# Optimization experiments

Hardware: AMD Instinct MI355X
Metric: run time of the kernel (lower is better)

The kernel has to match this reference:

```python
import jax, jax.numpy as jnp
import numpy as np

N, E, DIN, H, HEADS = 50000, 800000, 128, 64, 4


def setup_inputs() -> dict:
    key = jax.random.key(0)
    ks = jax.random.split(key, 12)

    def p(k, shape, fan_in):
        return jax.random.normal(k, shape, dtype=jnp.float32) / np.float32(np.sqrt(fan_in))

    return dict(
        x=jax.random.normal(ks[0], (N, DIN), dtype=jnp.float32),
        edge_index=jax.random.randint(ks[1], (2, E), 0, N, dtype=jnp.int32),
        # GCNConv(input_dim, hidden)
        W_gcn=p(ks[2], (DIN, H), DIN), b_gcn=jnp.zeros((H,), jnp.float32),
        # GATConv(hidden, hidden, heads=4, concat=True)
        W_gat=p(ks[3], (H, HEADS * H), H),
        att_src=p(ks[4], (HEADS, H), H), att_dst=p(ks[5], (HEADS, H), H),
        b_gat=jnp.zeros((HEADS * H,), jnp.float32),
        # SAGEConv(4*hidden, hidden): lin_l (neighbors, with bias), lin_r (root, no bias)
        W_sage_l=p(ks[6], (HEADS * H, H), HEADS * H), b_sage=jnp.zeros((H,), jnp.float32),
        W_sage_r=p(ks[7], (HEADS * H, H), HEADS * H),
        # edge-pair MLP: Linear(2*hidden, hidden) -> ReLU -> Linear(hidden, 1)
        W1=p(ks[8], (2 * H, H), 2 * H), b1=jnp.zeros((H,), jnp.float32),
        W2=p(ks[9], (H, 1), H), b2=jnp.zeros((1,), jnp.float32),
    )


def reference(x, edge_index, W_gcn, b_gcn, W_gat, att_src, att_dst, b_gat,
              W_sage_l, b_sage, W_sage_r, W1, b1, W2, b2):
    n = x.shape[0]
    src, dst = edge_index[0], edge_index[1]
    loop = jnp.arange(n, dtype=edge_index.dtype)
    # edges with self-loops appended (GCN and GAT add self-loops by default)
    s2 = jnp.concatenate([src, loop])
    d2 = jnp.concatenate([dst, loop])

    h = x @ W_gcn                                            # [N, H]
    deg = jax.ops.segment_sum(jnp.ones_like(d2, jnp.float32), d2, num_segments=n)
    dinv = jnp.where(deg > 0, jax.lax.rsqrt(jnp.maximum(deg, 1e-12)), 0.0)
    norm = dinv[s2] * dinv[d2]                               # [E+N]
    h = jax.ops.segment_sum(h[s2] * norm[:, None], d2, num_segments=n) + b_gcn
    h = jax.nn.relu(h)                                       # dropout: identity in eval

    # ---- GATConv (heads=4, concat=True, negative_slope=0.2) ----
    g = (h @ W_gat).reshape(n, HEADS, H)                     # [N, heads, C]
    a_s = jnp.sum(g * att_src, axis=-1)                      # [N, heads]
    a_d = jnp.sum(g * att_dst, axis=-1)
    e = jax.nn.leaky_relu(a_s[s2] + a_d[d2], 0.2)            # [E+N, heads]
    m = jax.ops.segment_max(e, d2, num_segments=n)           # per-target max (stable softmax)
    e = jnp.exp(e - m[d2])
    z = jax.ops.segment_sum(e, d2, num_segments=n)
    alpha = e / (z[d2] + 1e-16)                              # edge softmax over incoming edges
    g = jax.ops.segment_sum(g[s2] * alpha[:, :, None], d2, num_segments=n)
    g = jax.nn.relu(g.reshape(n, HEADS * H) + b_gat)

    # ---- SAGEConv (mean aggregation, root weight, no self-loops) ----
    nsum = jax.ops.segment_sum(g[src], dst, num_segments=n)
    cnt = jax.ops.segment_sum(jnp.ones_like(dst, jnp.float32), dst, num_segments=n)
    mean = nsum / jnp.maximum(cnt, 1.0)[:, None]
    s = jax.nn.relu(mean @ W_sage_l + b_sage + g @ W_sage_r)  # [N, H]

    # ---- edge-pair MLP + sigmoid ----
    ef = jnp.concatenate([s[src], s[dst]], axis=1)            # [E, 2H]
    pred = jax.nn.relu(ef @ W1 + b1) @ W2 + b2                # [E, 1]
    return jax.nn.sigmoid(pred[:, 0])
```

## Files before the change

### kernel.cpp

```cpp
#include <hip/hip_runtime.h>
#include <math.h>

typedef float v2f __attribute__((ext_vector_type(2)));
static __device__ __forceinline__ float4 f4s(float v){ return make_float4(v,v,v,v); }
static __device__ __forceinline__ float4 f4add(float4 a, float4 b){ return make_float4(a.x+b.x,a.y+b.y,a.z+b.z,a.w+b.w); }
static __device__ __forceinline__ float4 f4max(float4 a, float4 b){ return make_float4(fmaxf(a.x,b.x),fmaxf(a.y,b.y),fmaxf(a.z,b.z),fmaxf(a.w,b.w)); }
static __device__ __forceinline__ float4 f4scale(float4 a, float s){ return make_float4(a.x*s,a.y*s,a.z*s,a.w*s); }
static __device__ __forceinline__ float4 f4fma(float4 acc, float s, float4 b){
  acc.x += s*b.x; acc.y += s*b.y; acc.z += s*b.z; acc.w += s*b.w; return acc;
}
static __device__ __forceinline__ float4 f4relu(float4 a){ return f4max(a, f4s(0.f)); }
static __device__ __forceinline__ float4 f4leaky(float4 a){
  return make_float4(a.x>0.f?a.x:0.2f*a.x, a.y>0.f?a.y:0.2f*a.y, a.z>0.f?a.z:0.2f*a.z, a.w>0.f?a.w:0.2f*a.w);
}
static __device__ __forceinline__ float4 f4expf(float4 a){ return make_float4(__expf(a.x),__expf(a.y),__expf(a.z),__expf(a.w)); }
static __device__ __forceinline__ unsigned short f2bf(float f){
  unsigned int u = __float_as_uint(f);
  unsigned int r = (u + 0x7fffu + ((u >> 16) & 1u)) >> 16;
  return (unsigned short)r;
}
static __device__ __forceinline__ ushort4 f2bf4(float4 f){
  ushort4 r; r.x=f2bf(f.x); r.y=f2bf(f.y); r.z=f2bf(f.z); r.w=f2bf(f.w); return r;
}
static __device__ __forceinline__ float4 bfu2f4(uint2 u){
  return make_float4(__uint_as_float(u.x << 16), __uint_as_float(u.x & 0xffff0000u),
                     __uint_as_float(u.y << 16), __uint_as_float(u.y & 0xffff0000u));
}
static __device__ __forceinline__ float4 bfu2f4_lo(uint4 u){ return bfu2f4(make_uint2(u.x, u.y)); }
static __device__ __forceinline__ float4 bfu2f4_hi(uint4 u){ return bfu2f4(make_uint2(u.z, u.w)); }

typedef __attribute__((ext_vector_type(8))) unsigned short u16x8;
static __device__ __forceinline__ u16x8 f2bf8(float4 a, float4 b){
  u16x8 r;
  r[0]=f2bf(a.x); r[1]=f2bf(a.y); r[2]=f2bf(a.z); r[3]=f2bf(a.w);
  r[4]=f2bf(b.x); r[5]=f2bf(b.y); r[6]=f2bf(b.z); r[7]=f2bf(b.w);
  return r;
}
static __device__ __forceinline__ void red2(float4& a, float4& b){
  a.x += __shfl_xor(a.x, 8); a.y += __shfl_xor(a.y, 8);
  a.z += __shfl_xor(a.z, 8); a.w += __shfl_xor(a.w, 8);
  b.x += __shfl_xor(b.x, 8); b.y += __shfl_xor(b.y, 8);
  b.z += __shfl_xor(b.z, 8); b.w += __shfl_xor(b.w, 8);
}
static __device__ __forceinline__ unsigned char f2fp8(float v){
  return (unsigned char)(__builtin_amdgcn_cvt_pk_fp8_f32(v, v, 0, false) & 0xff);
}
static __device__ __forceinline__ unsigned int f4_fp8x4(float4 v){
  unsigned int r = __builtin_amdgcn_cvt_pk_fp8_f32(v.x, v.y, 0, false);
  r = __builtin_amdgcn_cvt_pk_fp8_f32(v.z, v.w, r, true);
  return r;
}
static __device__ __forceinline__ float4 fp8x4_f4(unsigned int q){
  v2f lo = __builtin_amdgcn_cvt_pk_f32_fp8(q, false);
  v2f hi = __builtin_amdgcn_cvt_pk_f32_fp8(q, true);
  return make_float4(lo[0], lo[1], hi[0], hi[1]);
}
static __device__ __forceinline__ float dot8(float4 a, float4 b, const float* v){
  return a.x*v[0]+a.y*v[1]+a.z*v[2]+a.w*v[3]+b.x*v[4]+b.y*v[5]+b.z*v[6]+b.w*v[7];
}

typedef __attribute__((ext_vector_type(8))) short bf16x8;
typedef __attribute__((ext_vector_type(4))) float f32x4;

__global__ __launch_bounds__(256) void k_rankw(const int* __restrict__ dst, int* __restrict__ cnt,
                                               int* __restrict__ rank, int E, int fb,
                                               const float* __restrict__ Wg, const float* __restrict__ Wl,
                                               const float* __restrict__ Wr, unsigned short* __restrict__ WT){
  if ((int)blockIdx.x < fb){
    int t = blockIdx.x*256 + threadIdx.x;
    if (t < E) rank[t] = atomicAdd(&cnt[dst[t]], 1);
    return;
  }
  int s = (blockIdx.x - fb)*256 + threadIdx.x;
  int l = s & 63, f = s >> 6;
  const float* wp; int ld;
  if (s < 2048){
    int cc = f & 15, kb = f >> 4;
    int c  = cc*16 + (l & 15);
    int kr = kb*32 + ((l >> 4) << 3);
    wp = Wg + (size_t)kr*256 + c; ld = 256;
  } else {
    int f2 = f - 32;
    int cc = f2 & 7, kb = f2 >> 3;
    int c  = cc*16 + (l & 15);
    int kr = kb*32 + ((l >> 4) << 3);
    wp = (c >= 64) ? (Wr + (size_t)kr*64 + (c - 64)) : (Wl + (size_t)kr*64 + c);
    ld = 64;
  }
  u16x8 o;
  #pragma unroll
  for (int j = 0; j < 8; ++j) o[j] = f2bf(wp[(size_t)j*ld]);
  *(u16x8*)(WT + (size_t)s*8) = o;
}

__global__ __launch_bounds__(256) void k_scan1v(const int* __restrict__ cnt, int* __restrict__ excl,
                                                int* __restrict__ bsum, int n, int nb,
                                                const float* __restrict__ Wg, const float* __restrict__ as,
                                                const float* __restrict__ ad, float* __restrict__ Vs,
                                                float* __restrict__ Vd){
  if ((int)blockIdx.x == nb){
    int t = threadIdx.x;
    int h = t >> 6, k = t & 63;
    float s = 0.f, d = 0.f;
    const float* wr = Wg + (size_t)k*256 + h*64;
    const float* ar = as + h*64;
    const float* dr = ad + h*64;
    for (int c = 0; c < 64; ++c){ float w = wr[c]; s += w*ar[c]; d += w*dr[c]; }
    Vs[t] = s; Vd[t] = d;
    return;
  }
  __shared__ int sc[256];
  int t = threadIdx.x; int i = blockIdx.x*256 + t;
  int v = (i<n)?cnt[i]:0;
  sc[t]=v; __syncthreads();
  for (int o=1;o<256;o<<=1){ int a=(t>=o)?sc[t-o]:0; __syncthreads(); sc[t]+=a; __syncthreads(); }
  if (i<n) excl[i] = sc[t]-v;
  if (t==255) bsum[blockIdx.x] = sc[t];
}
__global__ __launch_bounds__(256) void k_scan3b(const int* __restrict__ cnt, const int* __restrict__ excl,
                                                const int* __restrict__ bsum, int* __restrict__ offs,
                                                float* __restrict__ dinv, int n, int E, int nb){
  __shared__ int sb[256];
  int t = threadIdx.x;
  int v = (t<nb)?bsum[t]:0;
  sb[t]=v; __syncthreads();
  for (int o=1;o<256;o<<=1){ int a=(t>=o)?sb[t-o]:0; __syncthreads(); sb[t]+=a; __syncthreads(); }
  int bex = sb[blockIdx.x] - bsum[blockIdx.x];
  int i = blockIdx.x*256 + t;
  if (i < n){
    offs[i] = excl[i] + bex;
    dinv[i] = rsqrtf((float)cnt[i] + 1.0f);
    if (i == 0) offs[n] = E;
  }
}

__global__ __launch_bounds__(256) void k_fillg(const int* __restrict__ src, const int* __restrict__ dstv,
                                               const int* __restrict__ offs, const int* __restrict__ rank,
                                               int* __restrict__ csr, int E, int fb,
                                               const float* __restrict__ x, const float* __restrict__ Wg,
                                               unsigned char* __restrict__ a8, int n,
                                               const float* __restrict__ dinv){
  if ((int)blockIdx.x < fb){
    int t = blockIdx.x*256 + threadIdx.x;
    if (t < E) csr[offs[dstv[t]] + rank[t]] = src[t];
    return;
  }
  __shared__ unsigned short wb[1024*8];
  int tid = threadIdx.x;
  for (int s = tid; s < 1024; s += 256){
    int l = s & 63, f = s >> 6;
    int cc = f & 3, kb = f >> 2;
    int c  = cc*16 + (l & 15);
    int kr = kb*32 + ((l >> 4) << 3);
    const float* wp = Wg + (size_t)kr*64 + c;
    unsigned short* dp = &wb[s*8];
    #pragma unroll
    for (int j = 0; j < 8; ++j) dp[j] = f2bf(wp[(size_t)j*64]);
  }
  __syncthreads();
  int wv = tid >> 6, l = tid & 63;
  int lrow = l & 15;
  int lk = (l >> 4) << 3;
  int g = blockIdx.x - fb;
  int r0 = (g << 6) + (wv << 4);
  int m = r0 + lrow;
  bf16x8 afr[4];
  #pragma unroll
  for (int kb = 0; kb < 4; ++kb){
    bf16x8 a = {0,0,0,0,0,0,0,0};
    if (m < n){
      const float* p = x + (size_t)m*128 + kb*32 + lk;
      float4 f0 = *(const float4*)p;
      float4 f1 = *(const float4*)(p + 4);
      a[0]=(short)f2bf(f0.x); a[1]=(short)f2bf(f0.y); a[2]=(short)f2bf(f0.z); a[3]=(short)f2bf(f0.w);
      a[4]=(short)f2bf(f1.x); a[5]=(short)f2bf(f1.y); a[6]=(short)f2bf(f1.z); a[7]=(short)f2bf(f1.w);
    }
    afr[kb] = a;
  }
  int rbase = r0 + ((l >> 4) << 2);
  float sc[4];
  #pragma unroll
  for (int r = 0; r < 4; ++r) sc[r] = (rbase + r < n) ? dinv[rbase + r] : 0.f;
  #pragma unroll
  for (int cc = 0; cc < 4; ++cc){
    f32x4 acc = {0.f, 0.f, 0.f, 0.f};
    #pragma unroll
    for (int kb = 0; kb < 4; ++kb){
      bf16x8 b = *(const bf16x8*)&wb[((kb*4 + cc)*64 + l)*8];
      acc = __builtin_amdgcn_mfma_f32_16x16x32_bf16(afr[kb], b, acc, 0, 0, 0);
    }
    int c = cc*16 + lrow;
    #pragma unroll
    for (int r = 0; r < 4; ++r){
      int rr = rbase + r;
      if (rr < n) a8[(size_t)rr*64 + c] = f2fp8(acc[r] * sc[r]);
    }
  }
}

__global__ __launch_bounds__(256) void k_gcn(const unsigned char* __restrict__ a8, const float* __restrict__ dinv,
                                             const float* __restrict__ b, const int* __restrict__ offs,
                                             const int* __restrict__ csr, const float* __restrict__ Vs,
                                             const float* __restrict__ Vd, unsigned char* __restrict__ h8,
                                             float* __restrict__ D, int n){
  __shared__ float svs[256], svd[256];
  svs[threadIdx.x] = Vs[threadIdx.x];
  svd[threadIdx.x] = Vd[threadIdx.x];
  __syncthreads();
  int l = threadIdx.x & 63;
  int node = (((blockIdx.x*256 + threadIdx.x) >> 6) << 2) + (l >> 4);
  int l15 = l & 15;
  int grp = l15 >> 3, sub = l15 & 7;
  bool ok = node < n;
  int beg = 0, end = 0;
  float di = 0.f;
  if (ok){ beg = offs[node]; end = offs[node+1]; di = dinv[node]; }
  float4 aL0 = f4s(0.f), aH0 = f4s(0.f), aL1 = f4s(0.f), aH1 = f4s(0.f);
  int i = beg + grp;
  for (; i + 2 < end; i += 4){
    int s0 = csr[i], s1 = csr[i+2];
    uint2 u0 = *(const uint2*)(a8 + (size_t)s0*64 + (sub<<3));
    uint2 u1 = *(const uint2*)(a8 + (size_t)s1*64 + (sub<<3));
    aL0 = f4add(aL0, fp8x4_f4(u0.x)); aH0 = f4add(aH0, fp8x4_f4(u0.y));
    aL1 = f4add(aL1, fp8x4_f4(u1.x)); aH1 = f4add(aH1, fp8x4_f4(u1.y));
  }
  if (i < end){
    int s0 = csr[i];
    uint2 u0 = *(const uint2*)(a8 + (size_t)s0*64 + (sub<<3));
    aL0 = f4add(aL0, fp8x4_f4(u0.x)); aH0 = f4add(aH0, fp8x4_f4(u0.y));
  }
  float4 aL = f4add(aL0, aL1), aH = f4add(aH0, aH1);
  red2(aL, aH);
  if (ok){
    uint2 us = *(const uint2*)(a8 + (size_t)node*64 + (sub<<3));
    aL = f4add(aL, fp8x4_f4(us.x)); aH = f4add(aH, fp8x4_f4(us.y));
    float4 b0 = *(const float4*)(b + (sub<<3));
    float4 b1 = *(const float4*)(b + (sub<<3) + 4);
    float4 r0 = f4relu(f4fma(b0, di, aL));
    float4 r1 = f4relu(f4fma(b1, di, aH));
    if (grp == 0){
      uint2 q; q.x = f4_fp8x4(r0); q.y = f4_fp8x4(r1);
      *(uint2*)(h8 + (size_t)node*64 + (sub<<3)) = q;
    }
    const float* vs0 = svs + (grp*128) + (sub<<3);
    const float* vd0 = svd + (grp*128) + (sub<<3);
    float s0 = dot8(r0, r1, vs0);
    float s1 = dot8(r0, r1, vs0 + 64);
    float d0 = dot8(r0, r1, vd0);
    float d1 = dot8(r0, r1, vd0 + 64);
    #pragma unroll
    for (int o = 1; o < 8; o <<= 1){
      s0 += __shfl_xor(s0, o); s1 += __shfl_xor(s1, o);
      d0 += __shfl_xor(d0, o); d1 += __shfl_xor(d1, o);
    }
    if (sub == 0){
      *(float2*)(D + (size_t)node*8 + grp*2)     = make_float2(s0, s1);
      *(float2*)(D + (size_t)node*8 + 4 + grp*2) = make_float2(d0, d1);
    }
  }
}

#define GAT_CAP 128
__global__ __launch_bounds__(256) void k_gat2f(const float* __restrict__ D, const unsigned char* __restrict__ H8,
                                               const int* __restrict__ offs, const int* __restrict__ csr,
                                               const unsigned short* __restrict__ WT, const float* __restrict__ bg,
                                               unsigned short* __restrict__ R, unsigned char* __restrict__ P8, int n){
  __shared__ float wl[8][GAT_CAP*4];
  __shared__ int   sl[8][GAT_CAP];
  __shared__ unsigned short ytile[16][264];
  unsigned short* gtile = (unsigned short*)&wl[0][0];
  const unsigned short* WT1 = WT;
  const unsigned short* WT2 = WT + 2048*8;
  int tid = threadIdx.x;
  for (int s0 = tid; s0 < 8*264; s0 += 256) (&ytile[8][0])[s0] = 0;
  int hw = tid >> 5;
  int node = (blockIdx.x*256 + tid) >> 5;
  int l5 = tid & 31;
  int grp = l5 >> 4;
  int sub = l5 & 15;
  if (node < n){
    int beg = offs[node], end = offs[node+1];
    int deg = end - beg;
    float4 ed  = *(const float4*)(D + (size_t)node*8 + 4);
    float4 es0 = *(const float4*)(D + (size_t)node*8);
    float4 wself = f4expf(f4leaky(f4add(es0, ed)));
    float4 z4 = f4s(0.f);
    for (int i = beg + l5; i < end; i += 32){
      int s = csr[i];
      float4 w = f4expf(f4leaky(f4add(*(const float4*)(D + (size_t)s*8), ed)));
      int li = i - beg;
      if (li < GAT_CAP){ *(float4*)&wl[hw][li<<2] = w; sl[hw][li] = s << 6; }
      z4 = f4add(z4, w);
    }
    for (int m = 1; m < 32; m <<= 1){
      z4.x += __shfl_xor(z4.x, m); z4.y += __shfl_xor(z4.y, m);
      z4.z += __shfl_xor(z4.z, m); z4.w += __shfl_xor(z4.w, m);
    }
    z4 = f4add(z4, wself);
    int c0b = sub << 2;
    float4 a0 = f4s(0.f), a1 = f4s(0.f), a2 = f4s(0.f), a3 = f4s(0.f);
    int nl = deg < GAT_CAP ? deg : GAT_CAP;
    int i = grp;
    for (; i + 2 < nl; i += 4){
      int o0 = sl[hw][i], o1 = sl[hw][i+2];
      float4 w0 = *(const float4*)&wl[hw][i<<2];
      float4 w1 = *(const float4*)&wl[hw][(i+2)<<2];
      unsigned int q0 = *(const unsigned int*)(H8 + o0 + c0b);
      unsigned int q1 = *(const unsigned int*)(H8 + o1 + c0b);
      float4 f0 = fp8x4_f4(q0);
      float4 f1 = fp8x4_f4(q1);
      a0 = f4fma(a0, w0.x, f0); a1 = f4fma(a1, w0.y, f0);
      a2 = f4fma(a2, w0.z, f0); a3 = f4fma(a3, w0.w, f0);
      a0 = f4fma(a0, w1.x, f1); a1 = f4fma(a1, w1.y, f1);
      a2 = f4fma(a2, w1.z, f1); a3 = f4fma(a3, w1.w, f1);
    }
    if (i < nl){
      float4 w0 = *(const float4*)&wl[hw][i<<2];
      float4 f0 = fp8x4_f4(*(const unsigned int*)(H8 + sl[hw][i] + c0b));
      a0 = f4fma(a0, w0.x, f0); a1 = f4fma(a1, w0.y, f0);
      a2 = f4fma(a2, w0.z, f0); a3 = f4fma(a3, w0.w, f0);
    }
    for (int j = nl + grp; j < deg; j += 2){
      int s = csr[beg+j];
      float4 e = f4leaky(f4add(*(const float4*)(D + (size_t)s*8), ed));
      float4 w = f4expf(e);
      float4 f0 = fp8x4_f4(*(const unsigned int*)(H8 + ((size_t)s << 6) + c0b));
      a0 = f4fma(a0, w.x, f0); a1 = f4fma(a1, w.y, f0);
      a2 = f4fma(a2, w.z, f0); a3 = f4fma(a3, w.w, f0);
    }
    a0.x += __shfl_xor(a0.x, 16); a0.y += __shfl_xor(a0.y, 16); a0.z += __shfl_xor(a0.z, 16); a0.w += __shfl_xor(a0.w, 16);
    a1.x += __shfl_xor(a1.x, 16); a1.y += __shfl_xor(a1.y, 16); a1.z += __shfl_xor(a1.z, 16); a1.w += __shfl_xor(a1.w, 16);
    a2.x += __shfl_xor(a2.x, 16); a2.y += __shfl_xor(a2.y, 16); a2.z += __shfl_xor(a2.z, 16); a2.w += __shfl_xor(a2.w, 16);
    a3.x += __shfl_xor(a3.x, 16); a3.y += __shfl_xor(a3.y, 16); a3.z += __shfl_xor(a3.z, 16); a3.w += __shfl_xor(a3.w, 16);
    if (grp == 0){
      float4 fs = fp8x4_f4(*(const unsigned int*)(H8 + ((size_t)node << 6) + c0b));
      a0 = f4fma(a0, wself.x, fs);
      a1 = f4fma(a1, wself.y, fs);
      a2 = f4fma(a2, wself.z, fs);
      a3 = f4fma(a3, wself.w, fs);
      a0 = f4scale(a0, 1.f/(z4.x + 1e-16f));
      a1 = f4scale(a1, 1.f/(z4.y + 1e-16f));
      a2 = f4scale(a2, 1.f/(z4.z + 1e-16f));
      a3 = f4scale(a3, 1.f/(z4.w + 1e-16f));
      unsigned short* yp = &ytile[hw][sub << 2];
      *(ushort4*)(yp)       = f2bf4(a0);
      *(ushort4*)(yp + 64)  = f2bf4(a1);
      *(ushort4*)(yp + 128) = f2bf4(a2);
      *(ushort4*)(yp + 192) = f2bf4(a3);
    }
  } else if (grp == 0){
    ushort4 z = make_ushort4(0,0,0,0);
    unsigned short* yp = &ytile[hw][sub << 2];
    *(ushort4*)(yp)       = z;
    *(ushort4*)(yp + 64)  = z;
    *(ushort4*)(yp + 128) = z;
    *(ushort4*)(yp + 192) = z;
  }
  __syncthreads();
  int wv = tid >> 6, l = tid & 63;
  int lrow = l & 15;
  int lk = (l >> 4) << 3;
  int rbase4 = (l >> 4) << 2;
  bf16x8 af0 = *(const bf16x8*)&ytile[lrow][wv*64 + lk];
  bf16x8 af1 = *(const bf16x8*)&ytile[lrow][wv*64 + 32 + lk];
  #pragma unroll
  for (int q = 0; q < 4; ++q){
    int cc = wv*4 + q;
    f32x4 acc = {0.f, 0.f, 0.f, 0.f};
    acc = __builtin_amdgcn_mfma_f32_16x16x32_bf16(af0, *(const bf16x8*)&WT1[((size_t)((0*16 + cc)*64 + l))*8], acc, 0, 0, 0);
    acc = __builtin_amdgcn_mfma_f32_16x16x32_bf16(af1, *(const bf16x8*)&WT1[((size_t)((1*16 + cc)*64 + l))*8], acc, 0, 0, 0);
    int c = cc*16 + lrow;
    float bv = bg[c];
    #pragma unroll
    for (int r = 0; r < 4; ++r)
      gtile[(rbase4 + r)*264 + c] = f2bf(fmaxf(acc[r] + bv, 0.f));
  }
  __syncthreads();
  bf16x8 afb[8];
  #pragma unroll
  for (int kb = 0; kb < 8; ++kb)
    afb[kb] = *(const bf16x8*)&gtile[lrow*264 + kb*32 + lk];
  #pragma unroll
  for (int q = 0; q < 2; ++q){
    int cc = wv*2 + q;
    f32x4 acc = {0.f, 0.f, 0.f, 0.f};
    #pragma unroll
    for (int kb = 0; kb < 8; ++kb){
      bf16x8 b = *(const bf16x8*)&WT2[((size_t)((kb*8 + cc)*64 + l))*8];
      acc = __builtin_amdgcn_mfma_f32_16x16x32_bf16(afb[kb], b, acc, 0, 0, 0);
    }
    int c = cc*16 + lrow;
    #pragma unroll
    for (int r = 0; r < 4; ++r){
      int row = rbase4 + r;
      if (row < 8){
        int nd = blockIdx.x*8 + row;
        if (nd < n){
          float v = acc[r];
          if (c < 64) P8[(size_t)nd*64 + c] = f2fp8(v);
          else        R[(size_t)nd*64 + (c - 64)] = f2bf(v);
        }
      }
    }
  }
}

__global__ __launch_bounds__(256) void k_sage(const unsigned char* __restrict__ P8, const unsigned short* __restrict__ R,
                                              const float* __restrict__ b, const int* __restrict__ offs,
                                              const int* __restrict__ csr, const float* __restrict__ W1a,
                                              const float* __restrict__ W1b, unsigned char* __restrict__ T2, int n){
  __shared__ unsigned short wfr[1024*8];
  __shared__ unsigned short stile[16][72];
  int tid = threadIdx.x;
  for (int s = tid; s < 1024; s += 256){
    int l = s & 63, f = s >> 6;
    int cc = f & 7, kb = f >> 3;
    int c  = cc*16 + (l & 15);
    int kr = kb*32 + ((l >> 4) << 3);
    const float* wp = (c >= 64) ? (W1b + (size_t)kr*64 + (c - 64)) : (W1a + (size_t)kr*64 + c);
    unsigned short* dp = &wfr[s*8];
    #pragma unroll
    for (int j = 0; j < 8; ++j) dp[j] = f2bf(wp[(size_t)j*64]);
  }
  int wv = tid >> 6, l = tid & 63;
  int base = blockIdx.x*16;
  int lrow16 = (wv << 2) + (l >> 4);
  int node = base + lrow16;
  int l15 = l & 15;
  int grp = l15 >> 3, sub = l15 & 7;
  bool ok = node < n;
  int beg = 0, end = 0;
  if (ok){ beg = offs[node]; end = offs[node+1]; }
  float4 aL0 = f4s(0.f), aH0 = f4s(0.f), aL1 = f4s(0.f), aH1 = f4s(0.f);
  int i = beg + grp;
  for (; i + 2 < end; i += 4){
    int s0 = csr[i], s1 = csr[i+2];
    uint2 u0 = *(const uint2*)(P8 + (size_t)s0*64 + (sub<<3));
    uint2 u1 = *(const uint2*)(P8 + (size_t)s1*64 + (sub<<3));
    aL0 = f4add(aL0, fp8x4_f4(u0.x)); aH0 = f4add(aH0, fp8x4_f4(u0.y));
    aL1 = f4add(aL1, fp8x4_f4(u1.x)); aH1 = f4add(aH1, fp8x4_f4(u1.y));
  }
  if (i < end){
    int s0 = csr[i];
    uint2 u0 = *(const uint2*)(P8 + (size_t)s0*64 + (sub<<3));
    aL0 = f4add(aL0, fp8x4_f4(u0.x)); aH0 = f4add(aH0, fp8x4_f4(u0.y));
  }
  float4 aL = f4add(aL0, aL1), aH = f4add(aH0, aH1);
  red2(aL, aH);
  float4 r0 = f4s(0.f), r1 = f4s(0.f);
  if (ok){
    float minv = 1.f / fmaxf((float)(end - beg), 1.f);
    uint4 ur = *(const uint4*)(R + (size_t)node*64 + (sub<<3));
    float4 b0 = *(const float4*)(b + (sub<<3));
    float4 b1 = *(const float4*)(b + (sub<<3) + 4);
    r0 = f4relu(f4add(f4fma(b0, minv, aL), bfu2f4_lo(ur)));
    r1 = f4relu(f4add(f4fma(b1, minv, aH), bfu2f4_hi(ur)));
  }
  if (grp == 0) *(u16x8*)&stile[lrow16][sub << 3] = f2bf8(r0, r1);
  __syncthreads();
  int lrow = l & 15, lk = (l >> 4) << 3;
  bf16x8 af0 = *(const bf16x8*)&stile[lrow][lk];
  bf16x8 af1 = *(const bf16x8*)&stile[lrow][32 + lk];
  int rbase = (l >> 4) << 2;
  #pragma unroll
  for (int q = 0; q < 2; ++q){
    int cc = wv*2 + q;
    f32x4 acc = {0.f, 0.f, 0.f, 0.f};
    acc = __builtin_amdgcn_mfma_f32_16x16x32_bf16(af0, *(const bf16x8*)&wfr[(cc*64 + l)*8], acc, 0, 0, 0);
    acc = __builtin_amdgcn_mfma_f32_16x16x32_bf16(af1, *(const bf16x8*)&wfr[((8 + cc)*64 + l)*8], acc, 0, 0, 0);
    int c = cc*16 + lrow;
    #pragma unroll
    for (int r = 0; r < 4; ++r){
      int nd = base + rbase + r;
      if (nd < n) T2[(size_t)nd*128 + c] = f2fp8(acc[r]);
    }
  }
}

__global__ __launch_bounds__(256) void k_mlp(const unsigned char* __restrict__ T2,
                                             const float* __restrict__ b1, const float* __restrict__ W2,
                                             const float* __restrict__ b2, const int* __restrict__ src,
                                             const int* __restrict__ dst, float* __restrict__ out, int E){
  int t = threadIdx.x;
  int e = blockIdx.x*32 + (t >> 3);
  if (e >= E) return;
  int sub = t & 7;
  int s = src[e], d = dst[e];
  uint2 uu = *(const uint2*)(T2 + (size_t)s*128 + (sub<<3));
  uint2 vv = *(const uint2*)(T2 + (size_t)d*128 + 64 + (sub<<3));
  float4 u0 = fp8x4_f4(uu.x), u1 = fp8x4_f4(uu.y);
  float4 v0 = fp8x4_f4(vv.x), v1 = fp8x4_f4(vv.y);
  float4 bb0 = *(const float4*)(b1 + (sub<<3));
  float4 bb1 = *(const float4*)(b1 + (sub<<3) + 4);
  float4 w0 = *(const float4*)(W2 + (sub<<3));
  float4 w1 = *(const float4*)(W2 + (sub<<3) + 4);
  float4 ta = f4relu(f4add(f4add(u0, v0), bb0));
  float4 tb = f4relu(f4add(f4add(u1, v1), bb1));
  float p = ta.x*w0.x + ta.y*w0.y + ta.z*w0.z + ta.w*w0.w
          + tb.x*w1.x + tb.y*w1.y + tb.z*w1.z + tb.w*w1.w;
  p += __shfl_xor(p, 1);
  p += __shfl_xor(p, 2);
  p += __shfl_xor(p, 4);
  if (sub == 0) out[e] = 1.f / (1.f + __expf(-(p + b2[0])));
}

extern "C" void kernel_launch(void* const* d_in, const int* in_sizes, int n_in,
                              void* d_out, int out_size, void* d_ws, size_t ws_size,
                              hipStream_t stream){
  const float* x     = (const float*)d_in[0];
  const int*   eidx  = (const int*)  d_in[1];
  const float* W_gcn = (const float*)d_in[2];
  const float* b_gcn = (const float*)d_in[3];
  const float* W_gat = (const float*)d_in[4];
  const float* att_s = (const float*)d_in[5];
  const float* att_d = (const float*)d_in[6];
  const float* b_gat = (const float*)d_in[7];
  const float* W_sl  = (const float*)d_in[8];
  const float* b_sg  = (const float*)d_in[9];
  const float* W_sr  = (const float*)d_in[10];
  const float* W1    = (const float*)d_in[11];
  const float* b1    = (const float*)d_in[12];
  const float* W2    = (const float*)d_in[13];
  const float* b2    = (const float*)d_in[14];
  float* out = (float*)d_out;

  const int N = in_sizes[0] / 128;
  const int E = in_sizes[1] / 2;
  const int* src = eidx;
  const int* dst = eidx + E;

  float* ws   = (float*)d_ws;
  float* dinv = ws;
  float* D    = dinv + (size_t)N;
  float* Vs   = D + (size_t)N*8;
  float* Vd   = Vs + 256;
  unsigned short* WT = (unsigned short*)(Vd + 256);
  unsigned short* R  = WT + (size_t)6144*8;
  unsigned char*  A8 = (unsigned char*)(R + (size_t)N*64);
  unsigned char*  H8 = A8 + (size_t)N*64;
  unsigned char*  P8 = H8 + (size_t)N*64;
  unsigned char*  T2 = P8 + (size_t)N*64;
  int* cnt  = (int*)(T2 + (size_t)N*128);
  int* excl = cnt + N;
  int* bsum = excl + N;
  int* offs = bsum + 256;
  int* rank = offs + N + 1;
  int* csr  = rank + E;

  const int nb = (N + 255) / 256;
  const int fb = (E + 255) / 256;
  const int gtiles = (N + 63) / 64;
  const int nwb = (N + 15) / 16;

  hipMemsetAsync(cnt, 0, (size_t)N*sizeof(int), stream);
  k_rankw <<<fb + 24, 256, 0, stream>>>(dst, cnt, rank, E, fb, W_gat, W_sl, W_sr, WT);
  k_scan1v<<<nb + 1, 256, 0, stream>>>(cnt, excl, bsum, N, nb, W_gat, att_s, att_d, Vs, Vd);
  k_scan3b<<<nb, 256, 0, stream>>>(cnt, excl, bsum, offs, dinv, N, E, nb);
  k_fillg <<<fb + gtiles, 256, 0, stream>>>(src, dst, offs, rank, csr, E, fb,
                                            x, W_gcn, A8, N, dinv);

  k_gcn <<<nwb, 256, 0, stream>>>(A8, dinv, b_gcn, offs, csr, Vs, Vd, H8, D, N);

  k_gat2f<<<(N+7)/8, 256, 0, stream>>>(D, H8, offs, csr, WT, b_gat, R, P8, N);

  k_sage<<<nwb, 256, 0, stream>>>(P8, R, b_sg, offs, csr, W1, W1 + 64*64, T2, N);

  k_mlp <<<(E+31)/32, 256, 0, stream>>>(T2, b1, W2, b2, src, dst, out, E);
}
```

Before: 276.1 us.

## Process 32 nodes per GAT block to fill MFMA tiles and reuse weights

The fused GAT kernel now aggregates 32 nodes per block, with each half-wave handling four nodes in sequence, instead of 8. The two following MFMA projections then run on two full 16-row tiles rather than one half-padded tile. Each weight fragment loaded from global memory is reused across both tiles, and the zero-padding waste and per-block weight traffic drop by a factor of four. In exchange the grid has fewer blocks, the serialized aggregation makes each block longer, and the larger ytile plus extra register fragments may lower occupancy.

```diff
diff --git a/kernel.cpp b/kernel.cpp
--- a/kernel.cpp
+++ b/kernel.cpp
@@ -265,136 +265,153 @@
                                                const int* __restrict__ offs, const int* __restrict__ csr,
                                                const unsigned short* __restrict__ WT, const float* __restrict__ bg,
                                                unsigned short* __restrict__ R, unsigned char* __restrict__ P8, int n){
-  __shared__ float wl[8][GAT_CAP*4];
-  __shared__ int   sl[8][GAT_CAP];
-  __shared__ unsigned short ytile[16][264];
-  unsigned short* gtile = (unsigned short*)&wl[0][0];
+  __shared__ __align__(16) unsigned char smem_raw[8*GAT_CAP*4*4 + 8*GAT_CAP*4];
+  __shared__ unsigned short ytile[32][264];
+  float (*wl)[GAT_CAP*4] = reinterpret_cast<float (*)[GAT_CAP*4]>(smem_raw);
+  int   (*sl)[GAT_CAP]   = reinterpret_cast<int (*)[GAT_CAP]>(smem_raw + 8*GAT_CAP*4*4);
+  unsigned short* gtile  = reinterpret_cast<unsigned short*>(smem_raw);
   const unsigned short* WT1 = WT;
   const unsigned short* WT2 = WT + 2048*8;
   int tid = threadIdx.x;
-  for (int s0 = tid; s0 < 8*264; s0 += 256) (&ytile[8][0])[s0] = 0;
   int hw = tid >> 5;
-  int node = (blockIdx.x*256 + tid) >> 5;
   int l5 = tid & 31;
   int grp = l5 >> 4;
   int sub = l5 & 15;
-  if (node < n){
-    int beg = offs[node], end = offs[node+1];
-    int deg = end - beg;
-    float4 ed  = *(const float4*)(D + (size_t)node*8 + 4);
-    float4 es0 = *(const float4*)(D + (size_t)node*8);
-    float4 wself = f4expf(f4leaky(f4add(es0, ed)));
-    float4 z4 = f4s(0.f);
-    for (int i = beg + l5; i < end; i += 32){
-      int s = csr[i];
-      float4 w = f4expf(f4leaky(f4add(*(const float4*)(D + (size_t)s*8), ed)));
-      int li = i - beg;
-      if (li < GAT_CAP){ *(float4*)&wl[hw][li<<2] = w; sl[hw][li] = s << 6; }
-      z4 = f4add(z4, w);
-    }
-    for (int m = 1; m < 32; m <<= 1){
-      z4.x += __shfl_xor(z4.x, m); z4.y += __shfl_xor(z4.y, m);
-      z4.z += __shfl_xor(z4.z, m); z4.w += __shfl_xor(z4.w, m);
-    }
-    z4 = f4add(z4, wself);
-    int c0b = sub << 2;
-    float4 a0 = f4s(0.f), a1 = f4s(0.f), a2 = f4s(0.f), a3 = f4s(0.f);
-    int nl = deg < GAT_CAP ? deg : GAT_CAP;
-    int i = grp;
-    for (; i + 2 < nl; i += 4){
-      int o0 = sl[hw][i], o1 = sl[hw][i+2];
-      float4 w0 = *(const float4*)&wl[hw][i<<2];
-      float4 w1 = *(const float4*)&wl[hw][(i+2)<<2];
-      unsigned int q0 = *(const unsigned int*)(H8 + o0 + c0b);
-      unsigned int q1 = *(const unsigned int*)(H8 + o1 + c0b);
-      float4 f0 = fp8x4_f4(q0);
-      float4 f1 = fp8x4_f4(q1);
-      a0 = f4fma(a0, w0.x, f0); a1 = f4fma(a1, w0.y, f0);
-      a2 = f4fma(a2, w0.z, f0); a3 = f4fma(a3, w0.w, f0);
-      a0 = f4fma(a0, w1.x, f1); a1 = f4fma(a1, w1.y, f1);
-      a2 = f4fma(a2, w1.z, f1); a3 = f4fma(a3, w1.w, f1);
-    }
-    if (i < nl){
-      float4 w0 = *(const float4*)&wl[hw][i<<2];
-      float4 f0 = fp8x4_f4(*(const unsigned int*)(H8 + sl[hw][i] + c0b));
-      a0 = f4fma(a0, w0.x, f0); a1 = f4fma(a1, w0.y, f0);
-      a2 = f4fma(a2, w0.z, f0); a3 = f4fma(a3, w0.w, f0);
-    }
-    for (int j = nl + grp; j < deg; j += 2){
-      int s = csr[beg+j];
-      float4 e = f4leaky(f4add(*(const float4*)(D + (size_t)s*8), ed));
-      float4 w = f4expf(e);
-      float4 f0 = fp8x4_f4(*(const unsigned int*)(H8 + ((size_t)s << 6) + c0b));
-      a0 = f4fma(a0, w.x, f0); a1 = f4fma(a1, w.y, f0);
-      a2 = f4fma(a2, w.z, f0); a3 = f4fma(a3, w.w, f0);
-    }
-    a0.x += __shfl_xor(a0.x, 16); a0.y += __shfl_xor(a0.y, 16); a0.z += __shfl_xor(a0.z, 16); a0.w += __shfl_xor(a0.w, 16);
-    a1.x += __shfl_xor(a1.x, 16); a1.y += __shfl_xor(a1.y, 16); a1.z += __shfl_xor(a1.z, 16); a1.w += __shfl_xor(a1.w, 16);
-    a2.x += __shfl_xor(a2.x, 16); a2.y += __shfl_xor(a2.y, 16); a2.z += __shfl_xor(a2.z, 16); a2.w += __shfl_xor(a2.w, 16);
-    a3.x += __shfl_xor(a3.x, 16); a3.y += __shfl_xor(a3.y, 16); a3.z += __shfl_xor(a3.z, 16); a3.w += __shfl_xor(a3.w, 16);
-    if (grp == 0){
-      float4 fs = fp8x4_f4(*(const unsigned int*)(H8 + ((size_t)node << 6) + c0b));
-      a0 = f4fma(a0, wself.x, fs);
-      a1 = f4fma(a1, wself.y, fs);
-      a2 = f4fma(a2, wself.z, fs);
-      a3 = f4fma(a3, wself.w, fs);
-      a0 = f4scale(a0, 1.f/(z4.x + 1e-16f));
-      a1 = f4scale(a1, 1.f/(z4.y + 1e-16f));
-      a2 = f4scale(a2, 1.f/(z4.z + 1e-16f));
-      a3 = f4scale(a3, 1.f/(z4.w + 1e-16f));
-      unsigned short* yp = &ytile[hw][sub << 2];
-      *(ushort4*)(yp)       = f2bf4(a0);
-      *(ushort4*)(yp + 64)  = f2bf4(a1);
-      *(ushort4*)(yp + 128) = f2bf4(a2);
-      *(ushort4*)(yp + 192) = f2bf4(a3);
-    }
-  } else if (grp == 0){
-    ushort4 z = make_ushort4(0,0,0,0);
-    unsigned short* yp = &ytile[hw][sub << 2];
-    *(ushort4*)(yp)       = z;
-    *(ushort4*)(yp + 64)  = z;
-    *(ushort4*)(yp + 128) = z;
-    *(ushort4*)(yp + 192) = z;
+  for (int batch = 0; batch < 4; ++batch){
+    int lrow32 = batch*8 + hw;
+    int node = blockIdx.x*32 + lrow32;
+    if (node < n){
+      int beg = offs[node], end = offs[node+1];
+      int deg = end - beg;
+      float4 ed  = *(const float4*)(D + (size_t)node*8 + 4);
+      float4 es0 = *(const float4*)(D + (size_t)node*8);
+      float4 wself = f4expf(f4leaky(f4add(es0, ed)));
+      float4 z4 = f4s(0.f);
+      for (int i = beg + l5; i < end; i += 32){
+        int s = csr[i];
+        float4 w = f4expf(f4leaky(f4add(*(const float4*)(D + (size_t)s*8), ed)));
+        int li = i - beg;
+        if (li < GAT_CAP){ *(float4*)&wl[hw][li<<2] = w; sl[hw][li] = s << 6; }
+        z4 = f4add(z4, w);
+      }
+      for (int m = 1; m < 32; m <<= 1){
+        z4.x += __shfl_xor(z4.x, m); z4.y += __shfl_xor(z4.y, m);
+        z4.z += __shfl_xor(z4.z, m); z4.w += __shfl_xor(z4.w, m);
+      }
+      z4 = f4add(z4, wself);
+      int c0b = sub << 2;
+      float4 a0 = f4s(0.f), a1 = f4s(0.f), a2 = f4s(0.f), a3 = f4s(0.f);
+      int nl = deg < GAT_CAP ? deg : GAT_CAP;
+      int i = grp;
+      for (; i + 2 < nl; i += 4){
+        int o0 = sl[hw][i], o1 = sl[hw][i+2];
+        float4 w0 = *(const float4*)&wl[hw][i<<2];
+        float4 w1 = *(const float4*)&wl[hw][(i+2)<<2];
+        unsigned int q0 = *(const unsigned int*)(H8 + o0 + c0b);
+        unsigned int q1 = *(const unsigned int*)(H8 + o1 + c0b);
+        float4 f0 = fp8x4_f4(q0);
+        float4 f1 = fp8x4_f4(q1);
+        a0 = f4fma(a0, w0.x, f0); a1 = f4fma(a1, w0.y, f0);
+        a2 = f4fma(a2, w0.z, f0); a3 = f4fma(a3, w0.w, f0);
+        a0 = f4fma(a0, w1.x, f1); a1 = f4fma(a1, w1.y, f1);
+        a2 = f4fma(a2, w1.z, f1); a3 = f4fma(a3, w1.w, f1);
+      }
+      if (i < nl){
+        float4 w0 = *(const float4*)&wl[hw][i<<2];
+        float4 f0 = fp8x4_f4(*(const unsigned int*)(H8 + sl[hw][i] + c0b));
+        a0 = f4fma(a0, w0.x, f0); a1 = f4fma(a1, w0.y, f0);
+        a2 = f4fma(a2, w0.z, f0); a3 = f4fma(a3, w0.w, f0);
+      }
+      for (int j = nl + grp; j < deg; j += 2){
+        int s = csr[beg+j];
+        float4 e = f4leaky(f4add(*(const float4*)(D + (size_t)s*8), ed));
+        float4 w = f4expf(e);
+        float4 f0 = fp8x4_f4(*(const unsigned int*)(H8 + ((size_t)s << 6) + c0b));
+        a0 = f4fma(a0, w.x, f0); a1 = f4fma(a1, w.y, f0);
+        a2 = f4fma(a2, w.z, f0); a3 = f4fma(a3, w.w, f0);
+      }
+      a0.x += __shfl_xor(a0.x, 16); a0.y += __shfl_xor(a0.y, 16); a0.z += __shfl_xor(a0.z, 16); a0.w += __shfl_xor(a0.w, 16);
+      a1.x += __shfl_xor(a1.x, 16); a1.y += __shfl_xor(a1.y, 16); a1.z += __shfl_xor(a1.z, 16); a1.w += __shfl_xor(a1.w, 16);
+      a2.x += __shfl_xor(a2.x, 16); a2.y += __shfl_xor(a2.y, 16); a2.z += __shfl_xor(a2.z, 16); a2.w += __shfl_xor(a2.w, 16);
+      a3.x += __shfl_xor(a3.x, 16); a3.y += __shfl_xor(a3.y, 16); a3.z += __shfl_xor(a3.z, 16); a3.w += __shfl_xor(a3.w, 16);
+      if (grp == 0){
+        float4 fs = fp8x4_f4(*(const unsigned int*)(H8 + ((size_t)node << 6) + c0b));
+        a0 = f4fma(a0, wself.x, fs);
+        a1 = f4fma(a1, wself.y, fs);
+        a2 = f4fma(a2, wself.z, fs);
+        a3 = f4fma(a3, wself.w, fs);
+        a0 = f4scale(a0, 1.f/(z4.x + 1e-16f));
+        a1 = f4scale(a1, 1.f/(z4.y + 1e-16f));
+        a2 = f4scale(a2, 1.f/(z4.z + 1e-16f));
+        a3 = f4scale(a3, 1.f/(z4.w + 1e-16f));
+        unsigned short* yp = &ytile[lrow32][sub << 2];
+        *(ushort4*)(yp)       = f2bf4(a0);
+        *(ushort4*)(yp + 64)  = f2bf4(a1);
+        *(ushort4*)(yp + 128) = f2bf4(a2);
+        *(ushort4*)(yp + 192) = f2bf4(a3);
+      }
+    } else if (grp == 0){
+      ushort4 z = make_ushort4(0,0,0,0);
+      unsigned short* yp = &ytile[lrow32][sub << 2];
+      *(ushort4*)(yp)       = z;
+      *(ushort4*)(yp + 64)  = z;
+      *(ushort4*)(yp + 128) = z;
+      *(ushort4*)(yp + 192) = z;
+    }
   }
   __syncthreads();
   int wv = tid >> 6, l = tid & 63;
   int lrow = l & 15;
   int lk = (l >> 4) << 3;
   int rbase4 = (l >> 4) << 2;
-  bf16x8 af0 = *(const bf16x8*)&ytile[lrow][wv*64 + lk];
-  bf16x8 af1 = *(const bf16x8*)&ytile[lrow][wv*64 + 32 + lk];
+  bf16x8 afA[2][2];
+  #pragma unroll
+  for (int t = 0; t < 2; ++t){
+    afA[t][0] = *(const bf16x8*)&ytile[t*16 + lrow][wv*64 + lk];
+    afA[t][1] = *(const bf16x8*)&ytile[t*16 + lrow][wv*64 + 32 + lk];
+  }
   #pragma unroll
   for (int q = 0; q < 4; ++q){
     int cc = wv*4 + q;
-    f32x4 acc = {0.f, 0.f, 0.f, 0.f};
-    acc = __builtin_amdgcn_mfma_f32_16x16x32_bf16(af0, *(const bf16x8*)&WT1[((size_t)((0*16 + cc)*64 + l))*8], acc, 0, 0, 0);
-    acc = __builtin_amdgcn_mfma_f32_16x16x32_bf16(af1, *(const bf16x8*)&WT1[((size_t)((1*16 + cc)*64 + l))*8], acc, 0, 0, 0);
+    bf16x8 b0 = *(const bf16x8*)&WT1[((size_t)((0*16 + cc)*64 + l))*8];
+    bf16x8 b1 = *(const bf16x8*)&WT1[((size_t)((1*16 + cc)*64 + l))*8];
     int c = cc*16 + lrow;
     float bv = bg[c];
     #pragma unroll
-    for (int r = 0; r < 4; ++r)
-      gtile[(rbase4 + r)*264 + c] = f2bf(fmaxf(acc[r] + bv, 0.f));
+    for (int t = 0; t < 2; ++t){
+      f32x4 acc = {0.f, 0.f, 0.f, 0.f};
+      acc = __builtin_amdgcn_mfma_f32_16x16x32_bf16(afA[t][0], b0, acc, 0, 0, 0);
+      acc = __builtin_amdgcn_mfma_f32_16x16x32_bf16(afA[t][1], b1, acc, 0, 0, 0);
+      #pragma unroll
+      for (int r = 0; r < 4; ++r)
+        gtile[(t*16 + rbase4 + r)*264 + c] = f2bf(fmaxf(acc[r] + bv, 0.f));
+    }
   }
   __syncthreads();
-  bf16x8 afb[8];
-  #pragma unroll
-  for (int kb = 0; kb < 8; ++kb)
-    afb[kb] = *(const bf16x8*)&gtile[lrow*264 + kb*32 + lk];
+  bf16x8 afb[2][8];
+  #pragma unroll
+  for (int t = 0; t < 2; ++t)
+    #pragma unroll
+    for (int kb = 0; kb < 8; ++kb)
+      afb[t][kb] = *(const bf16x8*)&gtile[(t*16 + lrow)*264 + kb*32 + lk];
   #pragma unroll
   for (int q = 0; q < 2; ++q){
     int cc = wv*2 + q;
-    f32x4 acc = {0.f, 0.f, 0.f, 0.f};
+    f32x4 acc0 = {0.f, 0.f, 0.f, 0.f};
+    f32x4 acc1 = {0.f, 0.f, 0.f, 0.f};
     #pragma unroll
     for (int kb = 0; kb < 8; ++kb){
       bf16x8 b = *(const bf16x8*)&WT2[((size_t)((kb*8 + cc)*64 + l))*8];
-      acc = __builtin_amdgcn_mfma_f32_16x16x32_bf16(afb[kb], b, acc, 0, 0, 0);
+      acc0 = __builtin_amdgcn_mfma_f32_16x16x32_bf16(afb[0][kb], b, acc0, 0, 0, 0);
+      acc1 = __builtin_amdgcn_mfma_f32_16x16x32_bf16(afb[1][kb], b, acc1, 0, 0, 0);
     }
     int c = cc*16 + lrow;
     #pragma unroll
-    for (int r = 0; r < 4; ++r){
-      int row = rbase4 + r;
-      if (row < 8){
-        int nd = blockIdx.x*8 + row;
+    for (int t = 0; t < 2; ++t){
+      const f32x4& acc = t ? acc1 : acc0;
+      #pragma unroll
+      for (int r = 0; r < 4; ++r){
+        int nd = blockIdx.x*32 + t*16 + rbase4 + r;
         if (nd < n){
           float v = acc[r];
           if (c < 64) P8[(size_t)nd*64 + c] = f2fp8(v);
@@ -561,7 +578,7 @@
 
   k_gcn <<<nwb, 256, 0, stream>>>(A8, dinv, b_gcn, offs, csr, Vs, Vd, H8, D, N);
 
-  k_gat2f<<<(N+7)/8, 256, 0, stream>>>(D, H8, offs, csr, WT, b_gat, R, P8, N);
+  k_gat2f<<<(N+31)/32, 256, 0, stream>>>(D, H8, offs, csr, WT, b_gat, R, P8, N);
 
   k_sage<<<nwb, 256, 0, stream>>>(P8, R, b_sg, offs, csr, W1, W1 + 64*64, T2, N);
 
```

Measured after the change: 272.0 us. No clear change (-1.5%).
